# Kernel tuning notes

Measured on AMD Instinct MI355X. Metric: run time of the kernel, lower is better.

The kernel has to match this reference:

```python
import jax, jax.numpy as jnp
import numpy as np

N, E, IN_DIM, OUT_DIM, N_GRAPHS = 50000, 400000, 64, 128, 64


def setup_inputs() -> dict:
    key = jax.random.key(0)
    ks = jax.random.split(key, 16)
    x = jax.random.normal(ks[0], (N, IN_DIM), dtype=jnp.float32)
    edge_index = jax.random.randint(ks[1], (2, E), 0, N, dtype=jnp.int32)
    batch = jnp.sort(jax.random.randint(ks[2], (N,), 0, N_GRAPHS, dtype=jnp.int32))

    def glorot(k, shape):
        lim = np.sqrt(6.0 / (shape[0] + shape[1]))
        return jax.random.uniform(k, shape, jnp.float32, -lim, lim)

    d = IN_DIM
    return {
        "x": x, "edge_index": edge_index, "batch": batch,
        "W1": glorot(ks[3], (d, 2 * d)),     "b1": jnp.zeros((2 * d,), jnp.float32),
        "W2": glorot(ks[4], (2 * d, 4 * d)), "b2": jnp.zeros((4 * d,), jnp.float32),
        "W3": glorot(ks[5], (d, 2 * d)),     "b3": jnp.zeros((2 * d,), jnp.float32),
        "W4": glorot(ks[6], (2 * d, 4 * d)), "b4": jnp.zeros((4 * d,), jnp.float32),
        "W7": glorot(ks[7], (9 * d, OUT_DIM)), "b7": jnp.zeros((OUT_DIM,), jnp.float32),
    }


def _gcn_conv(x, W, b, src, dst, dis):
    # GCNConv: x' = D^{-1/2} (A + I) D^{-1/2} (x W) + b
    h = x @ W                                   # [N, F]
    norm = dis[src] * dis[dst]                  # [E]
    agg = jax.ops.segment_sum(h[src] * norm[:, None], dst, num_segments=N)
    agg = agg + h * (dis * dis)[:, None]        # self-loop contribution
    return agg + b


def reference(x, edge_index, batch, W1, b1, W2, b2, W3, b3, W4, b4, W7, b7):
    src, dst = edge_index[0], edge_index[1]
    # degree of A + I (PyG counts in-degree over columns, +1 for self-loop)
    deg = jax.ops.segment_sum(jnp.ones((E,), x.dtype), dst, num_segments=N) + 1.0
    dis = jax.lax.rsqrt(deg)

    i1 = jnp.tanh(_gcn_conv(x, W1, b1, src, dst, dis))
    i1 = jnp.tanh(_gcn_conv(i1, W2, b2, src, dst, dis))
    i1 = jax.ops.segment_max(i1, batch, num_segments=N_GRAPHS)  # global_max_pool
    i1 = jnp.max(i1, axis=0, keepdims=True)                     # [1, 4d]
    i1 = jnp.broadcast_to(i1, (x.shape[0], i1.shape[1]))        # expand to [N, 4d]

    i2 = jnp.tanh(_gcn_conv(x, W3, b3, src, dst, dis))
    i2 = jnp.tanh(_gcn_conv(i2, W4, b4, src, dst, dis))

    c = jnp.concatenate((i1, i2, x), axis=1)                    # [N, 9d]
    return jnp.tanh(_gcn_conv(c, W7, b7, src, dst, dis))
```

## Files before the change

kernel.cpp:

```cpp
#include <hip/hip_runtime.h>
#include <hip/hip_bf16.h>
#include <cstdint>
#include <cstddef>

#define NN 50000
#define EE 400000

typedef __attribute__((ext_vector_type(8))) __bf16 bf16x8;
typedef __attribute__((ext_vector_type(4))) float f32x4;

static __device__ __forceinline__ float dec_key(unsigned k) {
  return (k & 0x80000000u) ? __uint_as_float(k & 0x7fffffffu) : __uint_as_float(~k);
}
static __device__ __forceinline__ unsigned enc_key(float f) {
  unsigned b = __float_as_uint(f);
  return (f >= 0.f) ? (b | 0x80000000u) : ~b;
}

__global__ void count_kernel(const int* __restrict__ dst, int* __restrict__ cnt, int e) {
  int i = blockIdx.x * blockDim.x + threadIdx.x;
  if (i < e) atomicAdd(&cnt[dst[i]], 1);
}

__global__ void dis_kernel(const int* __restrict__ cnt, float* __restrict__ dis, int n) {
  int i = blockIdx.x * blockDim.x + threadIdx.x;
  if (i < n) dis[i] = rsqrtf((float)cnt[i] + 1.0f);
}

#define SCAN_CHUNK 1024
__global__ __launch_bounds__(256) void scan1_kernel(const int* __restrict__ cnt,
                                                    int* __restrict__ rowptr,
                                                    int* __restrict__ bsum, int n) {
  int b = blockIdx.x;
  int base = b * SCAN_CHUNK;
  int t = threadIdx.x;
  int v[4];
  int s = 0;
#pragma unroll
  for (int i = 0; i < 4; ++i) {
    int idx = base + t * 4 + i;
    v[i] = (idx < n) ? cnt[idx] : 0;
    s += v[i];
  }
  int lane = t & 63, w = t >> 6;
  int inc = s;
#pragma unroll
  for (int off = 1; off < 64; off <<= 1) {
    int o = __shfl_up(inc, off, 64);
    if (lane >= off) inc += o;
  }
  __shared__ int wsum[4];
  if (lane == 63) wsum[w] = inc;
  __syncthreads();
  int woff = 0;
  for (int i = 0; i < w; ++i) woff += wsum[i];
  int run = woff + inc - s;
#pragma unroll
  for (int i = 0; i < 4; ++i) {
    int idx = base + t * 4 + i;
    if (idx < n) rowptr[idx] = run;
    run += v[i];
  }
  if (t == 255) bsum[b] = woff + inc;
}

__global__ void scan2_kernel(int* __restrict__ bsum, int nb) {
  int t = threadIdx.x;
  int v = (t < nb) ? bsum[t] : 0;
  int s = v;
#pragma unroll
  for (int off = 1; off < 64; off <<= 1) {
    int o = __shfl_up(s, off, 64);
    if (t >= off) s += o;
  }
  if (t < nb) bsum[t] = s - v;
}

__global__ __launch_bounds__(256) void scan3_kernel(int* __restrict__ rowptr,
                                                    const int* __restrict__ bsum, int n, int total) {
  int i = blockIdx.x * blockDim.x + threadIdx.x;
  if (i < n) rowptr[i] += bsum[i >> 10];
  if (i == 0) rowptr[n] = total;
}

__global__ void fill_kernel(const int* __restrict__ src, const int* __restrict__ dst,
                            const int* __restrict__ rowptr, int* __restrict__ cursor,
                            int* __restrict__ col, int e) {
  int i = blockIdx.x * blockDim.x + threadIdx.x;
  if (i < e) {
    int d = dst[i];
    int p = atomicAdd(&cursor[d], 1);
    col[rowptr[d] + p] = src[i];
  }
}

__global__ __launch_bounds__(256) void wcvt_kernel(const float* __restrict__ W,
                                                   __bf16* __restrict__ Wt, int K, int Nout) {
  int idx = blockIdx.x * blockDim.x + threadIdx.x;
  if (idx < K * Nout) {
    int n = idx / K, k = idx - n * K;
    Wt[idx] = (__bf16)W[(size_t)k * Nout + n];
  }
}

#define BM 64
#define BN 64
#define BK 16

__global__ __launch_bounds__(256) void gemm_f32(
    const float* __restrict__ A, const float* __restrict__ W, float* __restrict__ C,
    int M, int K, int Nout, const float* __restrict__ colAdd, int accumulate, int doTanh) {
  __shared__ float As[BK][BM + 4];
  __shared__ float Ws[BK][BN];
  int tid = threadIdx.x;
  int row0 = blockIdx.x * BM;
  int col0 = blockIdx.y * BN;
  int tx = tid & 15;
  int ty = tid >> 4;
  float acc[4][4] = {};
  for (int k0 = 0; k0 < K; k0 += BK) {
#pragma unroll
    for (int i = 0; i < 4; ++i) {
      int idx = tid + i * 256;
      int r = idx >> 4, c = idx & 15;
      int gr = row0 + r;
      float v = (gr < M) ? A[(size_t)gr * K + k0 + c] : 0.f;
      As[c][r] = v;
    }
#pragma unroll
    for (int i = 0; i < 4; ++i) {
      int idx = tid + i * 256;
      int r = idx >> 6, c = idx & 63;
      Ws[r][c] = W[(size_t)(k0 + r) * Nout + col0 + c];
    }
    __syncthreads();
#pragma unroll
    for (int kk = 0; kk < BK; ++kk) {
      float4 av = *(const float4*)&As[kk][ty * 4];
      float4 wv = *(const float4*)&Ws[kk][tx * 4];
      float a[4] = {av.x, av.y, av.z, av.w};
      float w[4] = {wv.x, wv.y, wv.z, wv.w};
#pragma unroll
      for (int i = 0; i < 4; ++i)
#pragma unroll
        for (int j = 0; j < 4; ++j) acc[i][j] = fmaf(a[i], w[j], acc[i][j]);
    }
    __syncthreads();
  }
#pragma unroll
  for (int i = 0; i < 4; ++i) {
    int gr = row0 + ty * 4 + i;
    if (gr >= M) continue;
#pragma unroll
    for (int j = 0; j < 4; ++j) {
      int gc = col0 + tx * 4 + j;
      size_t idx = (size_t)gr * Nout + gc;
      float v = acc[i][j];
      if (colAdd) v += colAdd[gc];
      if (accumulate) v += C[idx];
      if (doTanh) v = tanhf(v);
      C[idx] = v;
    }
  }
}

#define TM 128
#define TN 64
#define TK 64

__global__ __launch_bounds__(256) void gemm_mfma(
    const __bf16* __restrict__ A, const __bf16* __restrict__ Wt,
    float* __restrict__ Cf, __bf16* __restrict__ Ch,
    int M, int K, int Nout, const float* __restrict__ colAdd, int doTanh,
    unsigned* __restrict__ colmaxOut) {
  __shared__ char lds[(TM * TK + TN * TK) * 2];
  char* AsB = lds;
  char* BtB = lds + TM * TK * 2;
  int tid = threadIdx.x;
  int row0 = blockIdx.x * TM;
  int col0 = blockIdx.y * TN;
  int w = tid >> 6, l = tid & 63;
  int lr = l & 15, lh = l >> 4;
  int wmB = (w >> 1) * 64;
  int wnB = (w & 1) * 32;
  f32x4 acc[4][2] = {};
  for (int k0 = 0; k0 < K; k0 += TK) {
    if (k0) __syncthreads();
#pragma unroll
    for (int i = 0; i < 4; ++i) {
      int id = tid + i * 256;
      int r = id >> 3, oc = id & 7;
      int gr = row0 + r;
      bf16x8 sv;
      if (gr < M) sv = *(const bf16x8*)(A + (size_t)gr * K + k0 + oc * 8);
      else sv = bf16x8{};
      int byte = (r * 128 + oc * 16) ^ ((r & 7) << 4);
      *(bf16x8*)(AsB + byte) = sv;
    }
#pragma unroll
    for (int i = 0; i < 2; ++i) {
      int id = tid + i * 256;
      int c = id >> 3, oc = id & 7;
      bf16x8 sv = *(const bf16x8*)(Wt + (size_t)(col0 + c) * K + k0 + oc * 8);
      int byte = (c * 128 + oc * 16) ^ ((c & 7) << 4);
      *(bf16x8*)(BtB + byte) = sv;
    }
    __syncthreads();
#pragma unroll
    for (int s = 0; s < 2; ++s) {
      bf16x8 af[4], bfr[2];
#pragma unroll
      for (int mi = 0; mi < 4; ++mi) {
        int r = wmB + mi * 16 + lr;
        int byte = (r * 128 + (s * 32 + lh * 8) * 2) ^ ((r & 7) << 4);
        af[mi] = *(const bf16x8*)(AsB + byte);
      }
#pragma unroll
      for (int ni = 0; ni < 2; ++ni) {
        int c = wnB + ni * 16 + lr;
        int byte = (c * 128 + (s * 32 + lh * 8) * 2) ^ ((c & 7) << 4);
        bfr[ni] = *(const bf16x8*)(BtB + byte);
      }
#pragma unroll
      for (int mi = 0; mi < 4; ++mi)
#pragma unroll
        for (int ni = 0; ni < 2; ++ni)
          acc[mi][ni] =
              __builtin_amdgcn_mfma_f32_16x16x32_bf16(af[mi], bfr[ni], acc[mi][ni], 0, 0, 0);
    }
  }
  float cmax[2] = {-2.0f, -2.0f};
#pragma unroll
  for (int mi = 0; mi < 4; ++mi) {
#pragma unroll
    for (int ni = 0; ni < 2; ++ni) {
#pragma unroll
      for (int r = 0; r < 4; ++r) {
        int gr = row0 + wmB + mi * 16 + lh * 4 + r;
        if (gr >= M) continue;
        int gc = col0 + wnB + ni * 16 + lr;
        size_t idx = (size_t)gr * Nout + gc;
        float v = acc[mi][ni][r];
        if (colAdd) v += colAdd[gc];
        if (doTanh) v = tanhf(v);
        if (colmaxOut) cmax[ni] = fmaxf(cmax[ni], v);
        if (Cf) Cf[idx] = v;
        if (Ch) Ch[idx] = (__bf16)v;
      }
    }
  }
  if (colmaxOut) {
#pragma unroll
    for (int ni = 0; ni < 2; ++ni) {
      float m = cmax[ni];
      m = fmaxf(m, __shfl_xor(m, 16));
      m = fmaxf(m, __shfl_xor(m, 32));
      if (lh == 0) {
        int gc = col0 + wnB + ni * 16 + lr;
        atomicMax(&colmaxOut[gc], enc_key(m));
      }
    }
  }
}

template <int F, bool EPI, typename OT>
__global__ __launch_bounds__(256) void agg_kernel(
    const float* __restrict__ H, const int* __restrict__ rowptr, const int* __restrict__ col,
    const float* __restrict__ dis, const float* __restrict__ bias, OT* __restrict__ out, int n) {
  constexpr int VEC = F / 64;
  int wid = (int)((blockIdx.x * blockDim.x + threadIdx.x) >> 6);
  int lane = threadIdx.x & 63;
  if (wid >= n) return;
  int node = __builtin_amdgcn_readfirstlane(wid);
  float dd = dis[node];
  float acc[VEC];
  {
    const float* hs = H + (size_t)node * F + lane * VEC;
    if constexpr (VEC == 4) {
      float4 h = *(const float4*)hs;
      acc[0] = h.x * dd * dd; acc[1] = h.y * dd * dd; acc[2] = h.z * dd * dd; acc[3] = h.w * dd * dd;
    } else if constexpr (VEC == 2) {
      float2 h = *(const float2*)hs;
      acc[0] = h.x * dd * dd; acc[1] = h.y * dd * dd;
    } else {
      acc[0] = hs[0] * dd * dd;
    }
  }
  int beg = rowptr[node], end = rowptr[node + 1];
  for (int e = beg; e < end; ++e) {
    int s = col[e];
    float w = dis[s] * dd;
    const float* hs = H + (size_t)s * F + lane * VEC;
    if constexpr (VEC == 4) {
      float4 h = *(const float4*)hs;
      acc[0] = fmaf(h.x, w, acc[0]); acc[1] = fmaf(h.y, w, acc[1]);
      acc[2] = fmaf(h.z, w, acc[2]); acc[3] = fmaf(h.w, w, acc[3]);
    } else if constexpr (VEC == 2) {
      float2 h = *(const float2*)hs;
      acc[0] = fmaf(h.x, w, acc[0]); acc[1] = fmaf(h.y, w, acc[1]);
    } else {
      acc[0] = fmaf(hs[0], w, acc[0]);
    }
  }
  OT* o = out + (size_t)node * F + lane * VEC;
#pragma unroll
  for (int i = 0; i < VEC; ++i) {
    float v = acc[i];
    if constexpr (EPI) v = tanhf(v + bias[lane * VEC + i]);
    o[i] = (OT)v;
  }
}

__global__ __launch_bounds__(128) void crow_kernel(const unsigned* __restrict__ maxkey,
                                                   const float* __restrict__ W7top,
                                                   float* __restrict__ crow) {
  int j = threadIdx.x;
  float s = 0.f;
  for (int f = 0; f < 256; ++f) s = fmaf(dec_key(maxkey[f]), W7top[f * 128 + j], s);
  crow[j] = s;
}

extern "C" void kernel_launch(void* const* d_in, const int* in_sizes, int n_in,
                              void* d_out, int out_size, void* d_ws, size_t ws_size,
                              hipStream_t stream) {
  const float* x  = (const float*)d_in[0];
  const int* ei   = (const int*)d_in[1];
  const int* srcp = ei;
  const int* dstp = ei + EE;
  const float* W1 = (const float*)d_in[3];
  const float* b1 = (const float*)d_in[4];
  const float* W2 = (const float*)d_in[5];
  const float* b2 = (const float*)d_in[6];
  const float* W3 = (const float*)d_in[7];
  const float* b3 = (const float*)d_in[8];
  const float* W4 = (const float*)d_in[9];
  const float* b4 = (const float*)d_in[10];
  const float* W7 = (const float*)d_in[11];
  const float* b7 = (const float*)d_in[12];
  float* out = (float*)d_out;

  char* p = (char*)d_ws;
  auto alloc = [&](size_t bytes) -> void* {
    void* r = (void*)p;
    p += (bytes + 255) & ~(size_t)255;
    return r;
  };
  float*  H   = (float*)alloc((size_t)NN * 128 * 4);
  float*  A   = (float*)alloc((size_t)NN * 128 * 4);
  __bf16* Hb  = (__bf16*)alloc((size_t)NN * 128 * 2);
  __bf16* Bb  = (__bf16*)alloc((size_t)NN * 256 * 2);
  float*  AX  = (float*)alloc((size_t)NN * 64 * 4);
  __bf16* W2t = (__bf16*)alloc((size_t)256 * 128 * 2);
  __bf16* W4t = (__bf16*)alloc((size_t)256 * 128 * 2);
  __bf16* W7t = (__bf16*)alloc((size_t)128 * 256 * 2);
  float* dis = (float*)alloc((size_t)NN * 4);
  int* cnt = (int*)alloc((size_t)NN * 4);
  int* cursor = (int*)alloc((size_t)NN * 4);
  int* rowptr = (int*)alloc((size_t)(NN + 1) * 4);
  int* col = (int*)alloc((size_t)EE * 4);
  int* bsum = (int*)alloc(64 * 4);
  unsigned* maxkey = (unsigned*)alloc(256 * 4);
  float* crow = (float*)alloc(128 * 4);

  hipMemsetAsync(cnt, 0, (size_t)NN * 4, stream);
  hipMemsetAsync(cursor, 0, (size_t)NN * 4, stream);
  hipMemsetAsync(maxkey, 0, 256 * 4, stream);

  int eb = (EE + 255) / 256;
  int nb = (NN + 255) / 256;
  int nchunks = (NN + SCAN_CHUNK - 1) / SCAN_CHUNK;
  count_kernel<<<eb, 256, 0, stream>>>(dstp, cnt, EE);
  dis_kernel<<<nb, 256, 0, stream>>>(cnt, dis, NN);
  scan1_kernel<<<nchunks, 256, 0, stream>>>(cnt, rowptr, bsum, NN);
  scan2_kernel<<<1, 64, 0, stream>>>(bsum, nchunks);
  scan3_kernel<<<nb, 256, 0, stream>>>(rowptr, bsum, NN, EE);
  fill_kernel<<<eb, 256, 0, stream>>>(srcp, dstp, rowptr, cursor, col, EE);

  wcvt_kernel<<<(256 * 128 + 255) / 256, 256, 0, stream>>>(W2, W2t, 128, 256);
  wcvt_kernel<<<(256 * 128 + 255) / 256, 256, 0, stream>>>(W4, W4t, 128, 256);
  wcvt_kernel<<<(128 * 256 + 255) / 256, 256, 0, stream>>>(W7 + 256 * 128, W7t, 256, 128);

  dim3 gB(256);
  int mrows = (NN + BM - 1) / BM;
  int mrowsT = (NN + TM - 1) / TM;
  int aggB = (NN + 3) / 4;

  agg_kernel<64, false, float><<<aggB, gB, 0, stream>>>(x, rowptr, col, dis, nullptr, AX, NN);
  gemm_f32<<<dim3(mrows, 2), gB, 0, stream>>>(AX, W1, A, NN, 64, 128, b1, 0, 1);
  agg_kernel<128, false, __bf16><<<aggB, gB, 0, stream>>>(A, rowptr, col, dis, nullptr, Hb, NN);
  gemm_mfma<<<dim3(mrowsT, 4), gB, 0, stream>>>(Hb, W2t, nullptr, nullptr, NN, 128, 256, b2, 1, maxkey);
  gemm_f32<<<dim3(mrows, 2), gB, 0, stream>>>(AX, W3, A, NN, 64, 128, b3, 0, 1);
  agg_kernel<128, false, __bf16><<<aggB, gB, 0, stream>>>(A, rowptr, col, dis, nullptr, Hb, NN);
  gemm_mfma<<<dim3(mrowsT, 4), gB, 0, stream>>>(Hb, W4t, nullptr, Bb, NN, 128, 256, b4, 1, nullptr);
  crow_kernel<<<1, 128, 0, stream>>>(maxkey, W7, crow);
  gemm_mfma<<<dim3(mrowsT, 2), gB, 0, stream>>>(Bb, W7t, H, nullptr, NN, 256, 128, crow, 0, nullptr);
  gemm_f32<<<dim3(mrows, 2), gB, 0, stream>>>(x, W7 + 512 * 128, H, NN, 64, 128, nullptr, 1, 0);
  agg_kernel<128, true, float><<<aggB, gB, 0, stream>>>(H, rowptr, col, dis, b7, out, NN);
}
```

Baseline: 477.4 us.

## Load MFMA operands directly from global memory, dropping LDS staging in GEMM

The bf16 MFMA GEMM no longer stages A and W tiles through shared memory with swizzling and barriers. Each lane now reads its bf16x8 fragments straight from global memory through per-row pointers, and the K loop is fully unrolled up to K=256 with out-of-range rows clamped. The goal is to remove LDS traffic and __syncthreads overhead for these small-K GEMMs. In exchange, each operand is re-read from global memory or cache by several waves, and the kernel now silently assumes K is at most 256.

```diff
diff --git a/kernel.cpp b/kernel.cpp
--- a/kernel.cpp
+++ b/kernel.cpp
@@ -166,16 +166,12 @@
 
 #define TM 128
 #define TN 64
-#define TK 64
 
 __global__ __launch_bounds__(256) void gemm_mfma(
     const __bf16* __restrict__ A, const __bf16* __restrict__ Wt,
     float* __restrict__ Cf, __bf16* __restrict__ Ch,
     int M, int K, int Nout, const float* __restrict__ colAdd, int doTanh,
     unsigned* __restrict__ colmaxOut) {
-  __shared__ char lds[(TM * TK + TN * TK) * 2];
-  char* AsB = lds;
-  char* BtB = lds + TM * TK * 2;
   int tid = threadIdx.x;
   int row0 = blockIdx.x * TM;
   int col0 = blockIdx.y * TN;
@@ -183,51 +179,34 @@
   int lr = l & 15, lh = l >> 4;
   int wmB = (w >> 1) * 64;
   int wnB = (w & 1) * 32;
+  const __bf16* arow[4];
+#pragma unroll
+  for (int mi = 0; mi < 4; ++mi) {
+    int r = row0 + wmB + mi * 16 + lr;
+    if (r >= M) r = M - 1;
+    arow[mi] = A + (size_t)r * K + lh * 8;
+  }
+  const __bf16* wrow[2];
+#pragma unroll
+  for (int ni = 0; ni < 2; ++ni) {
+    int c = col0 + wnB + ni * 16 + lr;
+    wrow[ni] = Wt + (size_t)c * K + lh * 8;
+  }
   f32x4 acc[4][2] = {};
-  for (int k0 = 0; k0 < K; k0 += TK) {
-    if (k0) __syncthreads();
-#pragma unroll
-    for (int i = 0; i < 4; ++i) {
-      int id = tid + i * 256;
-      int r = id >> 3, oc = id & 7;
-      int gr = row0 + r;
-      bf16x8 sv;
-      if (gr < M) sv = *(const bf16x8*)(A + (size_t)gr * K + k0 + oc * 8);
-      else sv = bf16x8{};
-      int byte = (r * 128 + oc * 16) ^ ((r & 7) << 4);
-      *(bf16x8*)(AsB + byte) = sv;
-    }
-#pragma unroll
-    for (int i = 0; i < 2; ++i) {
-      int id = tid + i * 256;
-      int c = id >> 3, oc = id & 7;
-      bf16x8 sv = *(const bf16x8*)(Wt + (size_t)(col0 + c) * K + k0 + oc * 8);
-      int byte = (c * 128 + oc * 16) ^ ((c & 7) << 4);
-      *(bf16x8*)(BtB + byte) = sv;
-    }
-    __syncthreads();
-#pragma unroll
-    for (int s = 0; s < 2; ++s) {
-      bf16x8 af[4], bfr[2];
-#pragma unroll
-      for (int mi = 0; mi < 4; ++mi) {
-        int r = wmB + mi * 16 + lr;
-        int byte = (r * 128 + (s * 32 + lh * 8) * 2) ^ ((r & 7) << 4);
-        af[mi] = *(const bf16x8*)(AsB + byte);
-      }
-#pragma unroll
-      for (int ni = 0; ni < 2; ++ni) {
-        int c = wnB + ni * 16 + lr;
-        int byte = (c * 128 + (s * 32 + lh * 8) * 2) ^ ((c & 7) << 4);
-        bfr[ni] = *(const bf16x8*)(BtB + byte);
-      }
-#pragma unroll
-      for (int mi = 0; mi < 4; ++mi)
-#pragma unroll
-        for (int ni = 0; ni < 2; ++ni)
-          acc[mi][ni] =
-              __builtin_amdgcn_mfma_f32_16x16x32_bf16(af[mi], bfr[ni], acc[mi][ni], 0, 0, 0);
-    }
+#pragma unroll
+  for (int ks = 0; ks < 8; ++ks) {
+    if (ks * 32 >= K) break;
+    bf16x8 af[4], bfr[2];
+#pragma unroll
+    for (int mi = 0; mi < 4; ++mi) af[mi] = *(const bf16x8*)(arow[mi] + ks * 32);
+#pragma unroll
+    for (int ni = 0; ni < 2; ++ni) bfr[ni] = *(const bf16x8*)(wrow[ni] + ks * 32);
+#pragma unroll
+    for (int mi = 0; mi < 4; ++mi)
+#pragma unroll
+      for (int ni = 0; ni < 2; ++ni)
+        acc[mi][ni] =
+            __builtin_amdgcn_mfma_f32_16x16x32_bf16(af[mi], bfr[ni], acc[mi][ni], 0, 0, 0);
   }
   float cmax[2] = {-2.0f, -2.0f};
 #pragma unroll
```

Measured after the change: 494.4 us. 1.04x slower.

## Merge the two branch first layers into one wide GEMM and aggregation

Applied to the files above, without the earlier changes.

Concatenates W1 and W3 (and their biases) into one 64x256 weight, so the first-layer GEMM of both branches runs as a single launch. The second-layer aggregation then runs once over 256 features instead of twice over 128, sharing the CSR index traffic. The max-pool branch skips tanh in its GEMM epilogue and applies tanh to the pooled maxima in crow_kernel instead, which is valid because tanh is monotonic. The cost is a wider fp32 intermediate and strided bf16 reads through a new lda parameter.

```diff
diff --git a/kernel.cpp b/kernel.cpp
--- a/kernel.cpp
+++ b/kernel.cpp
@@ -101,6 +101,20 @@
     int n = idx / K, k = idx - n * K;
     Wt[idx] = (__bf16)W[(size_t)k * Nout + n];
   }
+}
+
+__global__ __launch_bounds__(256) void wcat_kernel(const float* __restrict__ W1,
+                                                   const float* __restrict__ W3,
+                                                   const float* __restrict__ b1,
+                                                   const float* __restrict__ b3,
+                                                   float* __restrict__ Wcat,
+                                                   float* __restrict__ bcat) {
+  int idx = blockIdx.x * blockDim.x + threadIdx.x;
+  if (idx < 64 * 256) {
+    int k = idx >> 8, j = idx & 255;
+    Wcat[idx] = (j < 128) ? W1[k * 128 + j] : W3[k * 128 + (j - 128)];
+  }
+  if (idx < 256) bcat[idx] = (idx < 128) ? b1[idx] : b3[idx - 128];
 }
 
 #define BM 64
@@ -169,7 +183,7 @@
 #define TK 64
 
 __global__ __launch_bounds__(256) void gemm_mfma(
-    const __bf16* __restrict__ A, const __bf16* __restrict__ Wt,
+    const __bf16* __restrict__ A, int lda, const __bf16* __restrict__ Wt,
     float* __restrict__ Cf, __bf16* __restrict__ Ch,
     int M, int K, int Nout, const float* __restrict__ colAdd, int doTanh,
     unsigned* __restrict__ colmaxOut) {
@@ -192,7 +206,7 @@
       int r = id >> 3, oc = id & 7;
       int gr = row0 + r;
       bf16x8 sv;
-      if (gr < M) sv = *(const bf16x8*)(A + (size_t)gr * K + k0 + oc * 8);
+      if (gr < M) sv = *(const bf16x8*)(A + (size_t)gr * lda + k0 + oc * 8);
       else sv = bf16x8{};
       int byte = (r * 128 + oc * 16) ^ ((r & 7) << 4);
       *(bf16x8*)(AsB + byte) = sv;
@@ -229,7 +243,7 @@
               __builtin_amdgcn_mfma_f32_16x16x32_bf16(af[mi], bfr[ni], acc[mi][ni], 0, 0, 0);
     }
   }
-  float cmax[2] = {-2.0f, -2.0f};
+  float cmax[2] = {-3.0e38f, -3.0e38f};
 #pragma unroll
   for (int mi = 0; mi < 4; ++mi) {
 #pragma unroll
@@ -316,7 +330,7 @@
                                                    float* __restrict__ crow) {
   int j = threadIdx.x;
   float s = 0.f;
-  for (int f = 0; f < 256; ++f) s = fmaf(dec_key(maxkey[f]), W7top[f * 128 + j], s);
+  for (int f = 0; f < 256; ++f) s = fmaf(tanhf(dec_key(maxkey[f])), W7top[f * 128 + j], s);
   crow[j] = s;
 }
 
@@ -345,14 +359,16 @@
     p += (bytes + 255) & ~(size_t)255;
     return r;
   };
-  float*  H   = (float*)alloc((size_t)NN * 128 * 4);
-  float*  A   = (float*)alloc((size_t)NN * 128 * 4);
-  __bf16* Hb  = (__bf16*)alloc((size_t)NN * 128 * 2);
-  __bf16* Bb  = (__bf16*)alloc((size_t)NN * 256 * 2);
-  float*  AX  = (float*)alloc((size_t)NN * 64 * 4);
-  __bf16* W2t = (__bf16*)alloc((size_t)256 * 128 * 2);
-  __bf16* W4t = (__bf16*)alloc((size_t)256 * 128 * 2);
-  __bf16* W7t = (__bf16*)alloc((size_t)128 * 256 * 2);
+  float*  T13  = (float*)alloc((size_t)NN * 256 * 4);
+  float*  H    = (float*)alloc((size_t)NN * 128 * 4);
+  __bf16* Hb13 = (__bf16*)alloc((size_t)NN * 256 * 2);
+  __bf16* Bb   = (__bf16*)alloc((size_t)NN * 256 * 2);
+  float*  AX   = (float*)alloc((size_t)NN * 64 * 4);
+  __bf16* W2t  = (__bf16*)alloc((size_t)256 * 128 * 2);
+  __bf16* W4t  = (__bf16*)alloc((size_t)256 * 128 * 2);
+  __bf16* W7t  = (__bf16*)alloc((size_t)128 * 256 * 2);
+  float*  Wcat = (float*)alloc((size_t)64 * 256 * 4);
+  float*  bcat = (float*)alloc(256 * 4);
   float* dis = (float*)alloc((size_t)NN * 4);
   int* cnt = (int*)alloc((size_t)NN * 4);
   int* cursor = (int*)alloc((size_t)NN * 4);
@@ -379,6 +395,7 @@
   wcvt_kernel<<<(256 * 128 + 255) / 256, 256, 0, stream>>>(W2, W2t, 128, 256);
   wcvt_kernel<<<(256 * 128 + 255) / 256, 256, 0, stream>>>(W4, W4t, 128, 256);
   wcvt_kernel<<<(128 * 256 + 255) / 256, 256, 0, stream>>>(W7 + 256 * 128, W7t, 256, 128);
+  wcat_kernel<<<(64 * 256 + 255) / 256, 256, 0, stream>>>(W1, W3, b1, b3, Wcat, bcat);
 
   dim3 gB(256);
   int mrows = (NN + BM - 1) / BM;
@@ -386,14 +403,12 @@
   int aggB = (NN + 3) / 4;
 
   agg_kernel<64, false, float><<<aggB, gB, 0, stream>>>(x, rowptr, col, dis, nullptr, AX, NN);
-  gemm_f32<<<dim3(mrows, 2), gB, 0, stream>>>(AX, W1, A, NN, 64, 128, b1, 0, 1);
-  agg_kernel<128, false, __bf16><<<aggB, gB, 0, stream>>>(A, rowptr, col, dis, nullptr, Hb, NN);
-  gemm_mfma<<<dim3(mrowsT, 4), gB, 0, stream>>>(Hb, W2t, nullptr, nullptr, NN, 128, 256, b2, 1, maxkey);
-  gemm_f32<<<dim3(mrows, 2), gB, 0, stream>>>(AX, W3, A, NN, 64, 128, b3, 0, 1);
-  agg_kernel<128, false, __bf16><<<aggB, gB, 0, stream>>>(A, rowptr, col, dis, nullptr, Hb, NN);
-  gemm_mfma<<<dim3(mrowsT, 4), gB, 0, stream>>>(Hb, W4t, nullptr, Bb, NN, 128, 256, b4, 1, nullptr);
+  gemm_f32<<<dim3(mrows, 4), gB, 0, stream>>>(AX, Wcat, T13, NN, 64, 256, bcat, 0, 1);
+  agg_kernel<256, false, __bf16><<<aggB, gB, 0, stream>>>(T13, rowptr, col, dis, nullptr, Hb13, NN);
+  gemm_mfma<<<dim3(mrowsT, 4), gB, 0, stream>>>(Hb13, 256, W2t, nullptr, nullptr, NN, 128, 256, b2, 0, maxkey);
+  gemm_mfma<<<dim3(mrowsT, 4), gB, 0, stream>>>(Hb13 + 128, 256, W4t, nullptr, Bb, NN, 128, 256, b4, 1, nullptr);
   crow_kernel<<<1, 128, 0, stream>>>(maxkey, W7, crow);
-  gemm_mfma<<<dim3(mrowsT, 2), gB, 0, stream>>>(Bb, W7t, H, nullptr, NN, 256, 128, crow, 0, nullptr);
+  gemm_mfma<<<dim3(mrowsT, 2), gB, 0, stream>>>(Bb, 256, W7t, H, nullptr, NN, 256, 128, crow, 0, nullptr);
   gemm_f32<<<dim3(mrows, 2), gB, 0, stream>>>(x, W7 + 512 * 128, H, NN, 64, 128, nullptr, 1, 0);
   agg_kernel<128, true, float><<<aggB, gB, 0, stream>>>(H, rowptr, col, dis, b7, out, NN);
 }
```

After: 488.1 us. 1.02x slower.
